# Optimization experiments

Measured on AMD Instinct MI355X. Metric: run time of the kernel, lower is better.

Reference implementation:

```python
import jax, jax.numpy as jnp
import numpy as np

N = 4096
NFEAT = 512
NHID = 60
NCLASS = 4


def setup_inputs() -> dict:
    key = jax.random.key(0)
    ks = jax.random.split(key, 12)
    x = jax.random.normal(ks[0], (N, NFEAT), dtype=jnp.float32)
    # sparse-ish binary adjacency (sub_adj), symmetric not required by the module
    sub_adj = (jax.random.uniform(ks[1], (N, N)) < 0.002).astype(jnp.float32)
    # P_vec: init to ones (torch.sub in reset_parameters is non-inplace, so it stays ones)
    P_vec = jnp.ones((N * (N + 1) // 2,), dtype=jnp.float32)
    s1 = 1.0 / np.sqrt(NFEAT)
    s2 = 1.0 / np.sqrt(NHID)
    W1 = jax.random.normal(ks[2], (NFEAT, NHID), dtype=jnp.float32) * s1
    b1 = jax.random.normal(ks[3], (NHID,), dtype=jnp.float32) * 0.01
    W2 = jax.random.normal(ks[4], (NHID, NHID), dtype=jnp.float32) * s2
    b2 = jax.random.normal(ks[5], (NHID,), dtype=jnp.float32) * 0.01
    W3 = jax.random.normal(ks[6], (NHID, NHID), dtype=jnp.float32) * s2
    b3 = jax.random.normal(ks[7], (NHID,), dtype=jnp.float32) * 0.01
    lin_w = jax.random.normal(ks[8], (NHID, NCLASS), dtype=jnp.float32) * s2
    lin_b = jax.random.normal(ks[9], (NCLASS,), dtype=jnp.float32) * 0.01
    return {"x": x, "sub_adj": sub_adj, "P_vec": P_vec,
            "W1": W1, "b1": b1, "W2": W2, "b2": b2, "W3": W3, "b3": b3,
            "lin_w": lin_w, "lin_b": lin_b}


def reference(x, sub_adj, P_vec, W1, b1, W2, b2, W3, b3, lin_w, lin_b):
    n = sub_adj.shape[0]
    # scatter P_vec into lower triangle (incl. diagonal), then symmetrize
    il, jl = jnp.tril_indices(n)
    M = jnp.zeros((n, n), dtype=P_vec.dtype).at[il, jl].set(P_vec)
    P_hat_symm = M + M.T - jnp.diag(jnp.diag(M))
    # perturbed adjacency with self-loops
    A_tilde = jax.nn.sigmoid(P_hat_symm) * sub_adj + jnp.eye(n, dtype=P_vec.dtype)
    # degree (column sums, matching python sum(adj)); detached in the original
    d = jax.lax.stop_gradient(jnp.sum(A_tilde, axis=0))
    d_inv_sqrt = jnp.where(d > 0, d ** -0.5, 0.0)  # isinf -> 0
    # D^{-1/2} A D^{-1/2} without materializing diag matrices
    norm_adj = d_inv_sqrt[:, None] * A_tilde * d_inv_sqrt[None, :]
    # 3 GCN layers: spmm(norm_adj, x @ W) + b
    h1 = jax.nn.relu(norm_adj @ (x @ W1) + b1)
    h2 = jax.nn.relu(norm_adj @ (h1 @ W2) + b2)
    h3 = norm_adj @ (h2 @ W3) + b3
    logits = h3 @ lin_w + lin_b  # dropout is identity in eval / p=0
    return jax.nn.log_softmax(logits, axis=1)
```

## Files before the change

kernel.cpp:

```cpp
#include <hip/hip_runtime.h>
#include <math.h>

#define NN 4096
#define NFEAT 512
#define NHID 60
#define NCLASS 4
#define CAP 96
#define GSTRIDE 64

__global__ __launch_bounds__(256) void k_scan(const float* __restrict__ adj,
                                              const float* __restrict__ P,
                                              float* __restrict__ dcol,
                                              int* __restrict__ cnt,
                                              int* __restrict__ cols,
                                              float* __restrict__ vals) {
    const int base = blockIdx.x * 4096 + threadIdx.x;
    const float4* adj4 = (const float4*)adj;
    float4 a[16];
    #pragma unroll
    for (int u = 0; u < 16; ++u) a[u] = adj4[base + u * 256];
    float s = 0.f;
    #pragma unroll
    for (int u = 0; u < 16; ++u) s += (a[u].x + a[u].y) + (a[u].z + a[u].w);
    if (s == 0.f) return;
    #pragma unroll
    for (int u = 0; u < 16; ++u) {
        const float4 av4 = a[u];
        if (av4.x + av4.y + av4.z + av4.w == 0.f) continue;
        const float av[4] = {av4.x, av4.y, av4.z, av4.w};
        const int e0 = (base + u * 256) * 4;
        #pragma unroll
        for (int q = 0; q < 4; ++q) {
            if (av[q] != 0.f) {
                const int e = e0 + q;
                const int i = e >> 12;
                const int j = e & (NN - 1);
                const int hi = i > j ? i : j;
                const int lo = i > j ? j : i;
                const float pv = P[((hi * (hi + 1)) >> 1) + lo];
                const float s2 = av[q] / (1.f + __expf(-pv));
                atomicAdd(&dcol[j], s2);
                const int pos = atomicAdd(&cnt[i], 1);
                if (pos < CAP) { cols[i * CAP + pos] = j; vals[i * CAP + pos] = s2; }
            }
        }
    }
}

__global__ __launch_bounds__(256) void k_xw(const float* __restrict__ x,
                                            const float* __restrict__ W1,
                                            float* __restrict__ g1,
                                            float* __restrict__ dcol,
                                            int* __restrict__ cnt) {
    __shared__ float part[1024];
    const int tid = threadIdx.x;
    if (tid < 8) {
        const int z = blockIdx.x * 8 + tid;
        if (z < NN) dcol[z] = 0.f; else cnt[z - NN] = 0;
    }
    const int w = tid >> 6, lane = tid & 63;
    const int c = lane < NHID ? lane : 0;
    const int row0 = blockIdx.x * 4;
    const int k0 = w * (NFEAT / 4);
    const float* x0 = x + (row0 + 0) * NFEAT;
    const float* x1 = x + (row0 + 1) * NFEAT;
    const float* x2 = x + (row0 + 2) * NFEAT;
    const float* x3 = x + (row0 + 3) * NFEAT;
    float a0 = 0.f, a1 = 0.f, a2 = 0.f, a3 = 0.f;
    for (int k = k0; k < k0 + NFEAT / 4; k += 4) {
        const float4 xv0 = *(const float4*)(x0 + k);
        const float4 xv1 = *(const float4*)(x1 + k);
        const float4 xv2 = *(const float4*)(x2 + k);
        const float4 xv3 = *(const float4*)(x3 + k);
        const float w0 = W1[(k + 0) * NHID + c];
        const float w1 = W1[(k + 1) * NHID + c];
        const float w2 = W1[(k + 2) * NHID + c];
        const float w3 = W1[(k + 3) * NHID + c];
        a0 = fmaf(xv0.x, w0, fmaf(xv0.y, w1, fmaf(xv0.z, w2, fmaf(xv0.w, w3, a0))));
        a1 = fmaf(xv1.x, w0, fmaf(xv1.y, w1, fmaf(xv1.z, w2, fmaf(xv1.w, w3, a1))));
        a2 = fmaf(xv2.x, w0, fmaf(xv2.y, w1, fmaf(xv2.z, w2, fmaf(xv2.w, w3, a2))));
        a3 = fmaf(xv3.x, w0, fmaf(xv3.y, w1, fmaf(xv3.z, w2, fmaf(xv3.w, w3, a3))));
    }
    part[(w * 4 + 0) * 64 + lane] = a0;
    part[(w * 4 + 1) * 64 + lane] = a1;
    part[(w * 4 + 2) * 64 + lane] = a2;
    part[(w * 4 + 3) * 64 + lane] = a3;
    __syncthreads();
    const float o = part[(0 * 4 + w) * 64 + lane] + part[(1 * 4 + w) * 64 + lane]
                  + part[(2 * 4 + w) * 64 + lane] + part[(3 * 4 + w) * 64 + lane];
    g1[(row0 + w) * GSTRIDE + lane] = (lane < NHID) ? o : 0.f;
}

__device__ __forceinline__ float spmm_row(const float* __restrict__ gin,
                                          const float* __restrict__ dcol,
                                          const int* __restrict__ cnt,
                                          const int* __restrict__ cols,
                                          const float* __restrict__ vals,
                                          int i, int lane, float di) {
    const int nn = min(cnt[i], CAP);
    float acc = gin[i * GSTRIDE + lane] * di;
    const int4*   c4 = (const int4*)(cols + i * CAP);
    const float4* v4 = (const float4*)(vals + i * CAP);
    int e = 0;
    for (; e + 4 <= nn; e += 4) {
        const int4   jj = c4[e >> 2];
        const float4 vv = v4[e >> 2];
        const float f0 = vv.x * rsqrtf(1.f + dcol[jj.x]);
        const float f1 = vv.y * rsqrtf(1.f + dcol[jj.y]);
        const float f2 = vv.z * rsqrtf(1.f + dcol[jj.z]);
        const float f3 = vv.w * rsqrtf(1.f + dcol[jj.w]);
        const float g0 = gin[jj.x * GSTRIDE + lane];
        const float g1 = gin[jj.y * GSTRIDE + lane];
        const float g2 = gin[jj.z * GSTRIDE + lane];
        const float g3 = gin[jj.w * GSTRIDE + lane];
        acc = fmaf(f0, g0, fmaf(f1, g1, fmaf(f2, g2, fmaf(f3, g3, acc))));
    }
    for (; e < nn; ++e) {
        const int j = cols[i * CAP + e];
        const float f = vals[i * CAP + e] * rsqrtf(1.f + dcol[j]);
        acc = fmaf(f, gin[j * GSTRIDE + lane], acc);
    }
    return acc * di;
}

__global__ __launch_bounds__(256) void k_layer(const float* __restrict__ gin,
                                               float* __restrict__ gout,
                                               const float* __restrict__ dcol,
                                               const int* __restrict__ cnt,
                                               const int* __restrict__ cols,
                                               const float* __restrict__ vals,
                                               const float* __restrict__ bias,
                                               const float* __restrict__ W) {
    __shared__ float Ws[NHID * NHID];
    __shared__ float hs[256];
    const int tid = threadIdx.x;
    for (int t = tid; t < NHID * NHID; t += 256) Ws[t] = W[t];
    const int w = tid >> 6, lane = tid & 63;
    const int i = blockIdx.x * 4 + w;
    const float di = rsqrtf(1.f + dcol[i]);
    const float acc = spmm_row(gin, dcol, cnt, cols, vals, i, lane, di);
    hs[w * 64 + lane] = (lane < NHID) ? fmaxf(acc + bias[lane], 0.f) : 0.f;
    __syncthreads();
    const int c = lane < NHID ? lane : 0;
    float o = 0.f;
    #pragma unroll 6
    for (int k = 0; k < NHID; ++k)
        o = fmaf(hs[w * 64 + k], Ws[k * NHID + c], o);
    gout[i * GSTRIDE + lane] = (lane < NHID) ? o : 0.f;
}

__global__ __launch_bounds__(256) void k_final(const float* __restrict__ gin,
                                               float* __restrict__ out,
                                               const float* __restrict__ dcol,
                                               const int* __restrict__ cnt,
                                               const int* __restrict__ cols,
                                               const float* __restrict__ vals,
                                               const float* __restrict__ b3,
                                               const float* __restrict__ lw,
                                               const float* __restrict__ lb) {
    __shared__ float lws[NHID * NCLASS];
    __shared__ float hs[256];
    const int tid = threadIdx.x;
    for (int t = tid; t < NHID * NCLASS; t += 256) lws[t] = lw[t];
    const int w = tid >> 6, lane = tid & 63;
    const int i = blockIdx.x * 4 + w;
    const float di = rsqrtf(1.f + dcol[i]);
    const float acc = spmm_row(gin, dcol, cnt, cols, vals, i, lane, di);
    hs[w * 64 + lane] = (lane < NHID) ? acc + b3[lane] : 0.f;
    __syncthreads();
    if (lane < NCLASS) {
        float o = lb[lane];
        #pragma unroll 4
        for (int k = 0; k < NHID; ++k)
            o = fmaf(hs[w * 64 + k], lws[k * NCLASS + lane], o);
        float m = fmaxf(o, __shfl_xor(o, 1));
        m = fmaxf(m, __shfl_xor(m, 2));
        const float ex = __expf(o - m);
        float ss = ex + __shfl_xor(ex, 1);
        ss += __shfl_xor(ss, 2);
        out[i * NCLASS + lane] = o - m - __logf(ss);
    }
}

extern "C" void kernel_launch(void* const* d_in, const int* in_sizes, int n_in,
                              void* d_out, int out_size, void* d_ws, size_t ws_size,
                              hipStream_t stream) {
    const float* x   = (const float*)d_in[0];
    const float* adj = (const float*)d_in[1];
    const float* P   = (const float*)d_in[2];
    const float* W1  = (const float*)d_in[3];
    const float* b1  = (const float*)d_in[4];
    const float* W2  = (const float*)d_in[5];
    const float* b2  = (const float*)d_in[6];
    const float* W3  = (const float*)d_in[7];
    const float* b3  = (const float*)d_in[8];
    const float* lw  = (const float*)d_in[9];
    const float* lb  = (const float*)d_in[10];
    float* out = (float*)d_out;

    char* ws = (char*)d_ws;
    float* dcol = (float*)(ws);
    int*   cnt  = (int*)(ws + 16384);
    int*   cols = (int*)(ws + 32768);
    float* vals = (float*)(ws + 32768 + 1572864);
    float* bufA = (float*)(ws + 32768 + 2 * 1572864);
    float* bufB = (float*)(ws + 32768 + 2 * 1572864 + 1048576);

    k_xw   <<<NN / 4, 256, 0, stream>>>(x, W1, bufA, dcol, cnt);
    k_scan <<<NN * NN / 4 / 4096, 256, 0, stream>>>(adj, P, dcol, cnt, cols, vals);
    k_layer<<<NN / 4, 256, 0, stream>>>(bufA, bufB, dcol, cnt, cols, vals, b1, W2);
    k_layer<<<NN / 4, 256, 0, stream>>>(bufB, bufA, dcol, cnt, cols, vals, b2, W3);
    k_final<<<NN / 4, 256, 0, stream>>>(bufA, out, dcol, cnt, cols, vals, b3, lw, lb);
}
```

Baseline: 198.5 us.

## Compact nonzero adjacency chunks into per-wave shared queues before scanning

The adjacency scan now uses integer OR tests to find nonzero float4 chunks and pushes their indices into a per-wavefront shared-memory queue. All lanes then process the queued chunks together, so divergent sparse work no longer serializes whole wavefronts. Each block now covers half as many elements (8 loads per thread instead of 16), doubling the grid. The costs are shared-memory atomics, two block barriers, and re-reading each queued chunk from global memory.

```diff
diff --git a/kernel.cpp b/kernel.cpp
--- a/kernel.cpp
+++ b/kernel.cpp
@@ -7,6 +7,32 @@
 #define NCLASS 4
 #define CAP 96
 #define GSTRIDE 64
+#define QCAP 128
+
+__device__ __forceinline__ void scan_f4(const float4 av4, int f4idx,
+                                        const float* __restrict__ P,
+                                        float* __restrict__ dcol,
+                                        int* __restrict__ cnt,
+                                        int* __restrict__ cols,
+                                        float* __restrict__ vals) {
+    const float av[4] = {av4.x, av4.y, av4.z, av4.w};
+    const int e0 = f4idx * 4;
+    #pragma unroll
+    for (int q = 0; q < 4; ++q) {
+        if (av[q] != 0.f) {
+            const int e = e0 + q;
+            const int i = e >> 12;
+            const int j = e & (NN - 1);
+            const int hi = i > j ? i : j;
+            const int lo = i > j ? j : i;
+            const float pv = P[((hi * (hi + 1)) >> 1) + lo];
+            const float s = av[q] / (1.f + __expf(-pv));
+            atomicAdd(&dcol[j], s);
+            const int pos = atomicAdd(&cnt[i], 1);
+            if (pos < CAP) { cols[i * CAP + pos] = j; vals[i * CAP + pos] = s; }
+        }
+    }
+}
 
 __global__ __launch_bounds__(256) void k_scan(const float* __restrict__ adj,
                                               const float* __restrict__ P,
@@ -14,36 +40,36 @@
                                               int* __restrict__ cnt,
                                               int* __restrict__ cols,
                                               float* __restrict__ vals) {
-    const int base = blockIdx.x * 4096 + threadIdx.x;
-    const float4* adj4 = (const float4*)adj;
-    float4 a[16];
+    __shared__ int wq[4][QCAP];
+    __shared__ int wq_n[4];
+    const int tid = threadIdx.x;
+    const int w = tid >> 6, lane = tid & 63;
+    if (tid < 4) wq_n[tid] = 0;
+    __syncthreads();
+
+    const int base = blockIdx.x * 2048 + tid;
+    const uint4* adj4 = (const uint4*)adj;
+    uint4 a[8];
     #pragma unroll
-    for (int u = 0; u < 16; ++u) a[u] = adj4[base + u * 256];
-    float s = 0.f;
+    for (int u = 0; u < 8; ++u) a[u] = adj4[base + u * 256];
     #pragma unroll
-    for (int u = 0; u < 16; ++u) s += (a[u].x + a[u].y) + (a[u].z + a[u].w);
-    if (s == 0.f) return;
-    #pragma unroll
-    for (int u = 0; u < 16; ++u) {
-        const float4 av4 = a[u];
-        if (av4.x + av4.y + av4.z + av4.w == 0.f) continue;
-        const float av[4] = {av4.x, av4.y, av4.z, av4.w};
-        const int e0 = (base + u * 256) * 4;
-        #pragma unroll
-        for (int q = 0; q < 4; ++q) {
-            if (av[q] != 0.f) {
-                const int e = e0 + q;
-                const int i = e >> 12;
-                const int j = e & (NN - 1);
-                const int hi = i > j ? i : j;
-                const int lo = i > j ? j : i;
-                const float pv = P[((hi * (hi + 1)) >> 1) + lo];
-                const float s2 = av[q] / (1.f + __expf(-pv));
-                atomicAdd(&dcol[j], s2);
-                const int pos = atomicAdd(&cnt[i], 1);
-                if (pos < CAP) { cols[i * CAP + pos] = j; vals[i * CAP + pos] = s2; }
+    for (int u = 0; u < 8; ++u) {
+        if (a[u].x | a[u].y | a[u].z | a[u].w) {
+            const int p = atomicAdd(&wq_n[w], 1);
+            if (p < QCAP) wq[w][p] = base + u * 256;
+            else {
+                const uint4 v = a[u];
+                const float4 f = make_float4(__uint_as_float(v.x), __uint_as_float(v.y),
+                                             __uint_as_float(v.z), __uint_as_float(v.w));
+                scan_f4(f, base + u * 256, P, dcol, cnt, cols, vals);
             }
         }
+    }
+    __syncthreads();
+    const int n = min(wq_n[w], QCAP);
+    for (int l = lane; l < n; l += 64) {
+        const int idx = wq[w][l];
+        scan_f4(((const float4*)adj)[idx], idx, P, dcol, cnt, cols, vals);
     }
 }
 
@@ -207,7 +233,7 @@
     float* bufB = (float*)(ws + 32768 + 2 * 1572864 + 1048576);
 
     k_xw   <<<NN / 4, 256, 0, stream>>>(x, W1, bufA, dcol, cnt);
-    k_scan <<<NN * NN / 4 / 4096, 256, 0, stream>>>(adj, P, dcol, cnt, cols, vals);
+    k_scan <<<NN * NN / 4 / 2048, 256, 0, stream>>>(adj, P, dcol, cnt, cols, vals);
     k_layer<<<NN / 4, 256, 0, stream>>>(bufA, bufB, dcol, cnt, cols, vals, b1, W2);
     k_layer<<<NN / 4, 256, 0, stream>>>(bufB, bufA, dcol, cnt, cols, vals, b2, W3);
     k_final<<<NN / 4, 256, 0, stream>>>(bufA, out, dcol, cnt, cols, vals, b3, lw, lb);
```

Result: faster. 191.8 us (-3.3%).
